# Kernel tuning notes

Measured on AMD Instinct MI355X. Metric: run time of the kernel, lower is better.

## Reference

```python
import jax, jax.numpy as jnp
import numpy as np

N_NODES = 50000
N_EDGES = 800000
D = 128
N_GRAPHS = 64
EPS = 1e-5


def _bn(x, g, b):
    # BatchNorm1d training-mode statistics over the node/graph axis
    mu = x.mean(axis=0)
    var = x.var(axis=0)
    return g * (x - mu) / jnp.sqrt(var + EPS) + b


def setup_inputs() -> dict:
    key = jax.random.key(0)
    ks = jax.random.split(key, 32)
    s = 0.05
    inp = {
        'x': jax.random.normal(ks[0], (N_NODES, D), dtype=jnp.float32),
        'edge_index': jax.random.randint(ks[1], (2, N_EDGES), 0, N_NODES, dtype=jnp.int32),
        'batch': jnp.sort(jax.random.randint(ks[2], (N_NODES,), 0, N_GRAPHS, dtype=jnp.int32)),
        # stacked ResGatedGraphConv params for 3 layers (key/query/value/skip)
        'Wk': jax.random.normal(ks[3], (3, D, D)) * s,
        'bk': jnp.zeros((3, D)),
        'Wq': jax.random.normal(ks[4], (3, D, D)) * s,
        'bq': jnp.zeros((3, D)),
        'Wv': jax.random.normal(ks[5], (3, D, D)) * s,
        'bv': jnp.zeros((3, D)),
        'Ws': jax.random.normal(ks[6], (3, D, D)) * s,
        'bs': jnp.zeros((3, D)),
        # per-layer conv BatchNorm affine params
        'g_cl': jnp.ones((3, D)), 'b_cl': jnp.zeros((3, D)),
        # pool norms
        'g_gap': jnp.ones((D,)), 'b_gap': jnp.zeros((D,)),
        'g_gsp': jnp.ones((D,)), 'b_gsp': jnp.zeros((D,)),
        # MLP head: 2*D -> 256 -> 128 -> 5
        'W1': jax.random.normal(ks[7], (2 * D, 256)) * s, 'b1': jnp.zeros((256,)),
        'g1': jnp.ones((256,)), 'bt1': jnp.zeros((256,)),
        'W2': jax.random.normal(ks[8], (256, 128)) * s, 'b2': jnp.zeros((128,)),
        'g2': jnp.ones((128,)), 'bt2': jnp.zeros((128,)),
        'Wl': jax.random.normal(ks[9], (128, 5)) * s, 'bl': jnp.zeros((5,)),
    }
    return inp


def reference(x, edge_index, batch, Wk, bk, Wq, bq, Wv, bv, Ws, bs, g_cl, b_cl,
              g_gap, b_gap, g_gsp, b_gsp, W1, b1, g1, bt1, W2, b2, g2, bt2, Wl, bl):
    src, dst = edge_index[0], edge_index[1]
    n = x.shape[0]
    for i in range(3):
        k = x @ Wk[i] + bk[i]   # target-side gate term
        q = x @ Wq[i] + bq[i]   # source-side gate term
        v = x @ Wv[i] + bv[i]   # messages
        gate = jax.nn.sigmoid(k[dst] + q[src])          # [E, D]
        agg = jax.ops.segment_sum(gate * v[src], dst, num_segments=n)
        x = agg + x @ Ws[i] + bs[i]                      # residual skip
        x = jax.nn.relu(x)
        x = _bn(x, g_cl[i], b_cl[i])
        # dropout: identity in eval mode
    counts = jax.ops.segment_sum(jnp.ones((n,), x.dtype), batch, num_segments=N_GRAPHS)
    gap = jax.ops.segment_sum(x, batch, num_segments=N_GRAPHS) / jnp.maximum(counts, 1.0)[:, None]
    gsp = jax.ops.segment_max(x, batch, num_segments=N_GRAPHS)
    gsp = jnp.where(counts[:, None] > 0, gsp, 0.0)
    gap = _bn(gap, g_gap, b_gap)
    gsp = _bn(gsp, g_gsp, b_gsp)
    out = jnp.concatenate([gap, gsp], axis=1)            # [G, 2D]
    out = _bn(jax.nn.relu(out @ W1 + b1), g1, bt1)
    out = _bn(jax.nn.relu(out @ W2 + b2), g2, bt2)
    return out @ Wl + bl                                  # [G, 5]
```

## Files before the change

### kernel.cpp

```cpp
#include <hip/hip_runtime.h>
#include <math.h>

#define N_NODES 50000
#define N_PAD 50048
#define N_EDGES 800000
#define D 128
#define N_GRAPHS 64
#define EPS 1e-5f
#define PCHUNK 16
#define GSTRIPES 8
#define SCAN_NB 196
#define NEG_LOG2E (-1.4426950408889634f)

typedef __attribute__((ext_vector_type(8))) short bf16x8;
typedef __attribute__((ext_vector_type(4))) float f32x4;
typedef __attribute__((ext_vector_type(2))) _Float16 h16x2;

static inline size_t align256(size_t x) { return (x + 255) & ~(size_t)255; }

__device__ inline unsigned short f2bf(float x) {
    unsigned u = __builtin_bit_cast(unsigned, x);
    u += 0x7FFFu + ((u >> 16) & 1u);
    return (unsigned short)(u >> 16);
}
__device__ inline float bf2f(unsigned short h) {
    unsigned u = (unsigned)h << 16;
    return __builtin_bit_cast(float, u);
}
__device__ inline unsigned short f2h(float x) {
    _Float16 h = (_Float16)x;
    return __builtin_bit_cast(unsigned short, h);
}

__global__ void prep_w(const float* __restrict__ Wk, const float* __restrict__ Wq,
                       const float* __restrict__ Wv, const float* __restrict__ Ws,
                       unsigned short* __restrict__ Whi, unsigned short* __restrict__ Wlo)
{
    const int j = blockIdx.x & 127;
    const int mat = (blockIdx.x >> 7) & 3;
    const int layer = blockIdx.x >> 9;
    const int k = threadIdx.x;
    const float* Wsrc = (mat == 0) ? Wk : (mat == 1) ? Wq : (mat == 2) ? Wv : Ws;
    const float w = Wsrc[((size_t)layer * D + k) * D + j];
    const unsigned short hi = f2bf(w);
    const unsigned short lo = f2bf(w - bf2f(hi));
    const size_t o = (((size_t)layer * 4 + mat) * D + j) * D + k;
    Whi[o] = hi;
    Wlo[o] = lo;
}

__global__ void convert_bf16(const float* __restrict__ X, unsigned short* __restrict__ Xhi)
{
    const size_t idx = (size_t)blockIdx.x * blockDim.x + threadIdx.x;
    if (idx >= (size_t)N_PAD * (D / 4)) return;
    const size_t n = idx >> 5;
    float4 v = make_float4(0.f, 0.f, 0.f, 0.f);
    if (n < N_NODES) v = ((const float4*)X)[idx];
    ((ushort4*)Xhi)[idx] = make_ushort4(f2bf(v.x), f2bf(v.y), f2bf(v.z), f2bf(v.w));
}

__global__ void gemm_kqvs_mfma(
    const unsigned short* __restrict__ Xhi,
    const unsigned short* __restrict__ Whi, const unsigned short* __restrict__ Wlo,
    const float* __restrict__ bk, const float* __restrict__ bq,
    const float* __restrict__ bv, const float* __restrict__ bs,
    float* __restrict__ Kb, unsigned short* __restrict__ QVh, float* __restrict__ Sb)
{
    const int tid = threadIdx.x;
    const int wave = tid >> 6;
    const int pair = wave & 1;
    const int ct = (wave >> 1) + 4 * blockIdx.y;
    const int colbase = ct * 16;
    const int lane = tid & 63;
    const int l16 = lane & 15;
    const int lhi = lane >> 4;

    const int mA = pair ? 1 : 0;
    const int mB = pair ? 2 : 3;

    const size_t wbA = ((size_t)mA * D + colbase + l16) * D;
    const size_t wbB = ((size_t)mB * D + colbase + l16) * D;
    bf16x8 bhA[4], blA[4], bhB[4], blB[4];
    #pragma unroll
    for (int c = 0; c < 4; ++c) {
        bhA[c] = *(const bf16x8*)(Whi + wbA + c * 32 + lhi * 8);
        blA[c] = *(const bf16x8*)(Wlo + wbA + c * 32 + lhi * 8);
        bhB[c] = *(const bf16x8*)(Whi + wbB + c * 32 + lhi * 8);
        blB[c] = *(const bf16x8*)(Wlo + wbB + c * 32 + lhi * 8);
    }

    const float biasA = (pair ? bq : bk)[colbase + l16];
    const float biasB = (pair ? bv : bs)[colbase + l16];
    const int lc = colbase + l16;
    const int rbase = blockIdx.x * (16 * GSTRIPES);

    bf16x8 an[4];
    {
        const size_t arow = (size_t)(rbase + l16) * D;
        #pragma unroll
        for (int c = 0; c < 4; ++c) an[c] = *(const bf16x8*)(Xhi + arow + c * 32 + lhi * 8);
    }
    #pragma unroll
    for (int s = 0; s < GSTRIPES; ++s) {
        bf16x8 ah[4];
        #pragma unroll
        for (int c = 0; c < 4; ++c) ah[c] = an[c];
        if (s + 1 < GSTRIPES) {
            const size_t arow = (size_t)(rbase + (s + 1) * 16 + l16) * D;
            #pragma unroll
            for (int c = 0; c < 4; ++c) an[c] = *(const bf16x8*)(Xhi + arow + c * 32 + lhi * 8);
        }
        f32x4 accA = (f32x4){0.f, 0.f, 0.f, 0.f};
        f32x4 accB = (f32x4){0.f, 0.f, 0.f, 0.f};
        #pragma unroll
        for (int c = 0; c < 4; ++c) {
            accA = __builtin_amdgcn_mfma_f32_16x16x32_bf16(ah[c], bhA[c], accA, 0, 0, 0);
            accA = __builtin_amdgcn_mfma_f32_16x16x32_bf16(ah[c], blA[c], accA, 0, 0, 0);
            accB = __builtin_amdgcn_mfma_f32_16x16x32_bf16(ah[c], bhB[c], accB, 0, 0, 0);
            accB = __builtin_amdgcn_mfma_f32_16x16x32_bf16(ah[c], blB[c], accB, 0, 0, 0);
        }
        const int r0 = rbase + s * 16;
        if (pair == 0) {
            #pragma unroll
            for (int rgi = 0; rgi < 4; ++rgi) {
                const int row = r0 + lhi * 4 + rgi;
                if (row < N_NODES) {
                    Kb[(size_t)row * D + lc] = (accA[rgi] + biasA) * NEG_LOG2E;
                    Sb[(size_t)row * D + lc] = accB[rgi] + biasB;
                }
            }
        } else {
            unsigned int* qv32 = (unsigned int*)QVh;
            #pragma unroll
            for (int rgi = 0; rgi < 4; ++rgi) {
                const int row = r0 + lhi * 4 + rgi;
                if (row < N_NODES) {
                    const unsigned qh = f2h((accA[rgi] + biasA) * NEG_LOG2E);
                    const unsigned vh = f2h(accB[rgi] + biasB);
                    qv32[(size_t)row * D + lc] = qh | (vh << 16);
                }
            }
        }
    }
}

__global__ void hist_dst(const int* __restrict__ dst, int* __restrict__ cnt) {
    int e = blockIdx.x * blockDim.x + threadIdx.x;
    if (e < N_EDGES) atomicAdd(&cnt[dst[e]], 1);
}

__global__ void scan_block_sums(const int* __restrict__ cnt, int* __restrict__ bsum) {
    __shared__ int s[256];
    const int t = threadIdx.x;
    const int i = blockIdx.x * 256 + t;
    s[t] = (i < N_NODES) ? cnt[i] : 0;
    __syncthreads();
    #pragma unroll
    for (int off = 128; off > 0; off >>= 1) {
        if (t < off) s[t] += s[t + off];
        __syncthreads();
    }
    if (t == 0) bsum[blockIdx.x] = s[0];
}

__global__ void scan_block_offsets(const int* __restrict__ bsum, int* __restrict__ boff) {
    __shared__ int s[256];
    const int t = threadIdx.x;
    s[t] = (t < SCAN_NB) ? bsum[t] : 0;
    __syncthreads();
    for (int off = 1; off < 256; off <<= 1) {
        const int add = (t >= off) ? s[t - off] : 0;
        __syncthreads();
        s[t] += add;
        __syncthreads();
    }
    if (t < SCAN_NB) boff[t] = (t == 0) ? 0 : s[t - 1];
}

__global__ void scan_final(const int* __restrict__ cnt, const int* __restrict__ boff,
                           int* __restrict__ row_start, int* __restrict__ cursor) {
    __shared__ int s[256];
    const int t = threadIdx.x;
    const int i = blockIdx.x * 256 + t;
    const int v = (i < N_NODES) ? cnt[i] : 0;
    s[t] = v;
    __syncthreads();
    for (int off = 1; off < 256; off <<= 1) {
        const int add = (t >= off) ? s[t - off] : 0;
        __syncthreads();
        s[t] += add;
        __syncthreads();
    }
    if (i < N_NODES) {
        const int excl = boff[blockIdx.x] + s[t] - v;
        row_start[i] = excl;
        cursor[i] = excl;
    }
    if (i == N_NODES - 1) {
        row_start[N_NODES] = N_EDGES;
        cursor[N_NODES] = N_EDGES;
    }
}

__global__ void fill_csr(const int* __restrict__ src, const int* __restrict__ dst,
                         int* __restrict__ cursor, int* __restrict__ col) {
    int e = blockIdx.x * blockDim.x + threadIdx.x;
    if (e < N_EDGES) {
        int d = dst[e];
        int p = atomicAdd(&cursor[d], 1);
        col[p] = src[e];
    }
}

__global__ void aggregate(const float2* __restrict__ Kb2, const uint2* __restrict__ QV2,
                          const float2* __restrict__ Sb2,
                          const int* __restrict__ row_start, const int* __restrict__ col,
                          float2* __restrict__ H2)
{
    const int wave = threadIdx.x >> 6;
    const int node = blockIdx.x * 4 + wave;
    const unsigned lane = threadIdx.x & 63;
    const size_t nb = (size_t)node * 64 + lane;
    const float2 kd = Kb2[nb];
    const float2 sb = Sb2[nb];
    float acc0 = 0.f, acc1 = 0.f;
    const int e0 = __builtin_amdgcn_readfirstlane(row_start[node]);
    const int e1 = __builtin_amdgcn_readfirstlane(row_start[node + 1]);
    int e = e0;
    for (; e + 8 <= e1; e += 8) {
        unsigned off0 = (unsigned)col[e + 0] * 64u + lane;
        unsigned off1 = (unsigned)col[e + 1] * 64u + lane;
        unsigned off2 = (unsigned)col[e + 2] * 64u + lane;
        unsigned off3 = (unsigned)col[e + 3] * 64u + lane;
        unsigned off4 = (unsigned)col[e + 4] * 64u + lane;
        unsigned off5 = (unsigned)col[e + 5] * 64u + lane;
        unsigned off6 = (unsigned)col[e + 6] * 64u + lane;
        unsigned off7 = (unsigned)col[e + 7] * 64u + lane;
        const uint2 u0 = QV2[off0];
        const uint2 u1 = QV2[off1];
        const uint2 u2 = QV2[off2];
        const uint2 u3 = QV2[off3];
        const uint2 u4 = QV2[off4];
        const uint2 u5 = QV2[off5];
        const uint2 u6 = QV2[off6];
        const uint2 u7 = QV2[off7];
        #pragma unroll
        for (int j = 0; j < 8; ++j) {
            const uint2 u = (j == 0) ? u0 : (j == 1) ? u1 : (j == 2) ? u2 : (j == 3) ? u3
                          : (j == 4) ? u4 : (j == 5) ? u5 : (j == 6) ? u6 : u7;
            const h16x2 p0 = __builtin_bit_cast(h16x2, u.x);
            const h16x2 p1 = __builtin_bit_cast(h16x2, u.y);
            acc0 = fmaf(__builtin_amdgcn_rcpf(1.0f + exp2f(kd.x + (float)p0[0])), (float)p0[1], acc0);
            acc1 = fmaf(__builtin_amdgcn_rcpf(1.0f + exp2f(kd.y + (float)p1[0])), (float)p1[1], acc1);
        }
    }
    for (; e + 4 <= e1; e += 4) {
        unsigned off0 = (unsigned)col[e + 0] * 64u + lane;
        unsigned off1 = (unsigned)col[e + 1] * 64u + lane;
        unsigned off2 = (unsigned)col[e + 2] * 64u + lane;
        unsigned off3 = (unsigned)col[e + 3] * 64u + lane;
        const uint2 u0 = QV2[off0];
        const uint2 u1 = QV2[off1];
        const uint2 u2 = QV2[off2];
        const uint2 u3 = QV2[off3];
        #pragma unroll
        for (int j = 0; j < 4; ++j) {
            const uint2 u = (j == 0) ? u0 : (j == 1) ? u1 : (j == 2) ? u2 : u3;
            const h16x2 p0 = __builtin_bit_cast(h16x2, u.x);
            const h16x2 p1 = __builtin_bit_cast(h16x2, u.y);
            acc0 = fmaf(__builtin_amdgcn_rcpf(1.0f + exp2f(kd.x + (float)p0[0])), (float)p0[1], acc0);
            acc1 = fmaf(__builtin_amdgcn_rcpf(1.0f + exp2f(kd.y + (float)p1[0])), (float)p1[1], acc1);
        }
    }
    for (; e < e1; ++e) {
        const unsigned off = (unsigned)col[e] * 64u + lane;
        const uint2 u = QV2[off];
        const h16x2 p0 = __builtin_bit_cast(h16x2, u.x);
        const h16x2 p1 = __builtin_bit_cast(h16x2, u.y);
        acc0 = fmaf(__builtin_amdgcn_rcpf(1.0f + exp2f(kd.x + (float)p0[0])), (float)p0[1], acc0);
        acc1 = fmaf(__builtin_amdgcn_rcpf(1.0f + exp2f(kd.y + (float)p1[0])), (float)p1[1], acc1);
    }
    H2[nb] = make_float2(fmaxf(acc0 + sb.x, 0.0f), fmaxf(acc1 + sb.y, 0.0f));
}

__global__ void bn_stats(const float* __restrict__ H, float* __restrict__ fsum,
                         float* __restrict__ fsq)
{
    __shared__ float s1[256], s2[256];
    const int tid = threadIdx.x;
    const int d = tid & 127;
    const int rowoff = tid >> 7;
    float sum = 0.f, sq = 0.f;
    for (int n = blockIdx.x * 2 + rowoff; n < N_NODES; n += gridDim.x * 2) {
        const float v = H[(size_t)n * D + d];
        sum += v; sq += v * v;
    }
    s1[tid] = sum; s2[tid] = sq;
    __syncthreads();
    if (tid < 128) {
        atomicAdd(&fsum[d], s1[tid] + s1[tid + 128]);
        atomicAdd(&fsq[d],  s2[tid] + s2[tid + 128]);
    }
}

__global__ void bn_apply_fused(float* __restrict__ H, const float* __restrict__ fsum,
                               const float* __restrict__ fsq, const float* __restrict__ g,
                               const float* __restrict__ b,
                               unsigned short* __restrict__ Xhi, int write_bf)
{
    const int idx = blockIdx.x * blockDim.x + threadIdx.x;
    const int total = N_NODES * D / 4;
    if (idx >= total) return;
    float4 h = ((const float4*)H)[idx];
    float hv[4] = {h.x, h.y, h.z, h.w};
    const int dbase = (idx * 4) & 127;
    float o[4];
    #pragma unroll
    for (int c = 0; c < 4; ++c) {
        const int d = dbase + c;
        const float mu = fsum[d] * (1.0f / N_NODES);
        const float var = fsq[d] * (1.0f / N_NODES) - mu * mu;
        const float sc = g[d] * rsqrtf(var + EPS);
        o[c] = (hv[c] - mu) * sc + b[d];
    }
    ((float4*)H)[idx] = make_float4(o[0], o[1], o[2], o[3]);
    if (write_bf) {
        ((ushort4*)Xhi)[idx] = make_ushort4(f2bf(o[0]), f2bf(o[1]), f2bf(o[2]), f2bf(o[3]));
    }
}

__global__ void find_gstart(const int* __restrict__ batch, int* __restrict__ gstart) {
    const int g = threadIdx.x;
    if (g > N_GRAPHS) return;
    int lo = 0, hi = N_NODES;
    while (lo < hi) {
        int mid = (lo + hi) >> 1;
        if (batch[mid] < g) lo = mid + 1; else hi = mid;
    }
    gstart[g] = lo;
}

__global__ void pool_partial(const float* __restrict__ X, const int* __restrict__ gstart,
                             float* __restrict__ psum, float* __restrict__ pmax)
{
    const int g = blockIdx.x / PCHUNK;
    const int c = blockIdx.x % PCHUNK;
    const int d = threadIdx.x;
    const int lo = gstart[g], hi = gstart[g + 1];
    float sum = 0.f, mx = -INFINITY;
    for (int n = lo + c; n < hi; n += PCHUNK) {
        const float v = X[(size_t)n * D + d];
        sum += v;
        mx = fmaxf(mx, v);
    }
    psum[(size_t)blockIdx.x * D + d] = sum;
    pmax[(size_t)blockIdx.x * D + d] = mx;
}

__global__ void pool_combine(const float* __restrict__ psum, const float* __restrict__ pmax,
                             const int* __restrict__ gstart,
                             float* __restrict__ gap, float* __restrict__ gsp)
{
    const int g = blockIdx.x;
    const int d = threadIdx.x;
    float sum = 0.f, mx = -INFINITY;
    #pragma unroll
    for (int c = 0; c < PCHUNK; ++c) {
        sum += psum[(size_t)(g * PCHUNK + c) * D + d];
        mx = fmaxf(mx, pmax[(size_t)(g * PCHUNK + c) * D + d]);
    }
    const int cnt = gstart[g + 1] - gstart[g];
    gap[g * D + d] = sum / fmaxf((float)cnt, 1.0f);
    gsp[g * D + d] = (cnt > 0) ? mx : 0.0f;
}

__global__ void bn_rows(const float* __restrict__ A, int rows, int cols,
                        const float* __restrict__ g, const float* __restrict__ b,
                        float* __restrict__ out, int out_cols, int out_off)
{
    const int c = blockIdx.x * blockDim.x + threadIdx.x;
    if (c >= cols) return;
    float sum = 0.f, sq = 0.f;
    for (int r = 0; r < rows; ++r) {
        const float v = A[r * cols + c];
        sum += v; sq += v * v;
    }
    const float mu = sum / rows;
    const float var = sq / rows - mu * mu;
    const float sc = g[c] * rsqrtf(var + EPS);
    const float sh = b[c] - mu * sc;
    for (int r = 0; r < rows; ++r) {
        out[r * out_cols + out_off + c] = A[r * cols + c] * sc + sh;
    }
}

__global__ void gemm_small(const float* __restrict__ A, const float* __restrict__ W,
                           const float* __restrict__ bias, float* __restrict__ out,
                           int K, int C, int relu)
{
    __shared__ float as[256];
    const int r = blockIdx.x;
    for (int k = threadIdx.x; k < K; k += blockDim.x) as[k] = A[r * K + k];
    __syncthreads();
    const int j = threadIdx.x;
    if (j < C) {
        float acc = bias[j];
        for (int k = 0; k < K; ++k) acc = fmaf(as[k], W[k * C + j], acc);
        if (relu) acc = fmaxf(acc, 0.f);
        out[r * C + j] = acc;
    }
}

extern "C" void kernel_launch(void* const* d_in, const int* in_sizes, int n_in,
                              void* d_out, int out_size, void* d_ws, size_t ws_size,
                              hipStream_t stream)
{
    const float* x     = (const float*)d_in[0];
    const int*   ei    = (const int*)d_in[1];
    const int*   srcE  = ei;
    const int*   dstE  = ei + N_EDGES;
    const int*   batch = (const int*)d_in[2];
    const float* Wk = (const float*)d_in[3];  const float* bk = (const float*)d_in[4];
    const float* Wq = (const float*)d_in[5];  const float* bq = (const float*)d_in[6];
    const float* Wv = (const float*)d_in[7];  const float* bv = (const float*)d_in[8];
    const float* Ws = (const float*)d_in[9];  const float* bs = (const float*)d_in[10];
    const float* g_cl = (const float*)d_in[11]; const float* b_cl = (const float*)d_in[12];
    const float* g_gap = (const float*)d_in[13]; const float* b_gap = (const float*)d_in[14];
    const float* g_gsp = (const float*)d_in[15]; const float* b_gsp = (const float*)d_in[16];
    const float* W1 = (const float*)d_in[17]; const float* b1 = (const float*)d_in[18];
    const float* g1 = (const float*)d_in[19]; const float* bt1 = (const float*)d_in[20];
    const float* W2 = (const float*)d_in[21]; const float* b2 = (const float*)d_in[22];
    const float* g2 = (const float*)d_in[23]; const float* bt2 = (const float*)d_in[24];
    const float* Wl = (const float*)d_in[25]; const float* bl = (const float*)d_in[26];
    float* out = (float*)d_out;

    char* ws = (char*)d_ws;
    size_t off = 0;
    const size_t bufB = (size_t)N_NODES * D * sizeof(float);
    float* Kb = (float*)(ws + off); off = align256(off + bufB);
    unsigned short* QVh = (unsigned short*)(ws + off); off = align256(off + bufB);
    float* Sb = (float*)(ws + off); off = align256(off + bufB);
    float* H  = (float*)(ws + off); off = align256(off + bufB);
    unsigned short* Xhi = (unsigned short*)(ws + off); off = align256(off + (size_t)N_PAD * D * 2);
    unsigned short* Whi = (unsigned short*)(ws + off); off = align256(off + (size_t)12 * D * D * 2);
    unsigned short* Wlo = (unsigned short*)(ws + off); off = align256(off + (size_t)12 * D * D * 2);
    float* fsum = (float*)(ws + off); off = align256(off + 128 * sizeof(float));
    float* fsq  = (float*)(ws + off); off = align256(off + 128 * sizeof(float));
    int* cnt       = (int*)(ws + off); off = align256(off + (size_t)N_NODES * sizeof(int));
    int* row_start = (int*)(ws + off); off = align256(off + (size_t)(N_NODES + 1) * sizeof(int));
    int* cursor    = (int*)(ws + off); off = align256(off + (size_t)(N_NODES + 1) * sizeof(int));
    int* colI      = (int*)(ws + off); off = align256(off + (size_t)N_EDGES * sizeof(int));
    int* bsum      = (int*)(ws + off); off = align256(off + 256 * sizeof(int));
    int* boff      = (int*)(ws + off); off = align256(off + 256 * sizeof(int));
    int* gstart    = (int*)(ws + off); off = align256(off + (N_GRAPHS + 1) * sizeof(int));
    float* psum = (float*)(ws + off); off = align256(off + (size_t)N_GRAPHS * PCHUNK * D * sizeof(float));
    float* pmax = (float*)(ws + off); off = align256(off + (size_t)N_GRAPHS * PCHUNK * D * sizeof(float));
    float* gap = (float*)(ws + off); off = align256(off + (size_t)N_GRAPHS * D * sizeof(float));
    float* gsp = (float*)(ws + off); off = align256(off + (size_t)N_GRAPHS * D * sizeof(float));
    float* h0  = (float*)(ws + off); off = align256(off + (size_t)N_GRAPHS * 256 * sizeof(float));
    float* h1  = (float*)(ws + off); off = align256(off + (size_t)N_GRAPHS * 256 * sizeof(float));
    float* h2  = (float*)(ws + off); off = align256(off + (size_t)N_GRAPHS * 128 * sizeof(float));
    if (off > ws_size) return;

    hipMemsetAsync(cnt, 0, (size_t)N_NODES * sizeof(int), stream);
    hist_dst<<<(N_EDGES + 255) / 256, 256, 0, stream>>>(dstE, cnt);
    scan_block_sums<<<SCAN_NB, 256, 0, stream>>>(cnt, bsum);
    scan_block_offsets<<<1, 256, 0, stream>>>(bsum, boff);
    scan_final<<<SCAN_NB, 256, 0, stream>>>(cnt, boff, row_start, cursor);
    fill_csr<<<(N_EDGES + 255) / 256, 256, 0, stream>>>(srcE, dstE, cursor, colI);
    find_gstart<<<1, 128, 0, stream>>>(batch, gstart);
    prep_w<<<12 * 128, 128, 0, stream>>>(Wk, Wq, Wv, Ws, Whi, Wlo);
    convert_bf16<<<(N_PAD * (D / 4) + 255) / 256, 256, 0, stream>>>(x, Xhi);

    for (int i = 0; i < 3; ++i) {
        gemm_kqvs_mfma<<<dim3(N_PAD / (16 * GSTRIPES), 2), 512, 0, stream>>>(
            Xhi,
            Whi + (size_t)i * 4 * D * D, Wlo + (size_t)i * 4 * D * D,
            bk + i * D, bq + i * D, bv + i * D, bs + i * D,
            Kb, QVh, Sb);
        aggregate<<<N_NODES / 4, 256, 0, stream>>>(
            (const float2*)Kb, (const uint2*)QVh, (const float2*)Sb, row_start, colI, (float2*)H);
        hipMemsetAsync(fsum, 0, 128 * sizeof(float), stream);
        hipMemsetAsync(fsq, 0, 128 * sizeof(float), stream);
        bn_stats<<<256, 256, 0, stream>>>(H, fsum, fsq);
        bn_apply_fused<<<(N_NODES * D / 4 + 255) / 256, 256, 0, stream>>>(
            H, fsum, fsq, g_cl + i * D, b_cl + i * D, Xhi, (i < 2) ? 1 : 0);
    }

    pool_partial<<<N_GRAPHS * PCHUNK, 128, 0, stream>>>(H, gstart, psum, pmax);
    pool_combine<<<N_GRAPHS, 128, 0, stream>>>(psum, pmax, gstart, gap, gsp);
    bn_rows<<<1, 128, 0, stream>>>(gap, N_GRAPHS, 128, g_gap, b_gap, h0, 256, 0);
    bn_rows<<<1, 128, 0, stream>>>(gsp, N_GRAPHS, 128, g_gsp, b_gsp, h0, 256, 128);

    gemm_small<<<N_GRAPHS, 256, 0, stream>>>(h0, W1, b1, h1, 256, 256, 1);
    bn_rows<<<1, 256, 0, stream>>>(h1, N_GRAPHS, 256, g1, bt1, h1, 256, 0);
    gemm_small<<<N_GRAPHS, 256, 0, stream>>>(h1, W2, b2, h2, 256, 128, 1);
    bn_rows<<<1, 128, 0, stream>>>(h2, N_GRAPHS, 128, g2, bt2, h2, 128, 0);
    gemm_small<<<N_GRAPHS, 256, 0, stream>>>(h2, Wl, bl, out, 128, 5, 0);
}
```

Baseline: 731.0 us.

## Split wave into half-waves processing two edges per gather with 16-byte loads

The aggregate kernel now has each half-wave (32 lanes) handle a different source edge, with each lane gathering a 16-byte packed K/Q/V slice covering four feature dims instead of 8 bytes for two. The partial sums from the two halves are combined with a cross-half shuffle before the skip add and ReLU. bn_stats is also vectorised to float4 loads with a deeper shared-memory reduction. The intent is to halve the number of gather instructions and widen memory transactions, at the cost of extra shuffles, an odd-edge tail where the upper half-wave sits idle, and more registers per lane.

```diff
diff --git a/kernel.cpp b/kernel.cpp
--- a/kernel.cpp
+++ b/kernel.cpp
@@ -212,94 +212,107 @@
     }
 }
 
-__global__ void aggregate(const float2* __restrict__ Kb2, const uint2* __restrict__ QV2,
-                          const float2* __restrict__ Sb2,
+__global__ void aggregate(const float4* __restrict__ Kb4, const uint4* __restrict__ QV4,
+                          const float4* __restrict__ Sb4,
                           const int* __restrict__ row_start, const int* __restrict__ col,
-                          float2* __restrict__ H2)
+                          float4* __restrict__ H4)
 {
     const int wave = threadIdx.x >> 6;
     const int node = blockIdx.x * 4 + wave;
     const unsigned lane = threadIdx.x & 63;
-    const size_t nb = (size_t)node * 64 + lane;
-    const float2 kd = Kb2[nb];
-    const float2 sb = Sb2[nb];
-    float acc0 = 0.f, acc1 = 0.f;
+    const unsigned l31 = lane & 31;
+    const bool hi = lane >= 32;
+    const size_t nb = (size_t)node * 32 + l31;
+    const float4 kd = Kb4[nb];
+    float a0 = 0.f, a1 = 0.f, a2 = 0.f, a3 = 0.f;
     const int e0 = __builtin_amdgcn_readfirstlane(row_start[node]);
     const int e1 = __builtin_amdgcn_readfirstlane(row_start[node + 1]);
     int e = e0;
+
+#define AGG_DIM(u, comp, kdc, acc)                                              \
+    {                                                                           \
+        const h16x2 p = __builtin_bit_cast(h16x2, (u).comp);                    \
+        acc = fmaf(__builtin_amdgcn_rcpf(1.0f + exp2f(kdc + (float)p[0])),      \
+                   (float)p[1], acc);                                           \
+    }
+#define AGG_EDGE(u) AGG_DIM(u, x, kd.x, a0) AGG_DIM(u, y, kd.y, a1) \
+                    AGG_DIM(u, z, kd.z, a2) AGG_DIM(u, w, kd.w, a3)
+
     for (; e + 8 <= e1; e += 8) {
-        unsigned off0 = (unsigned)col[e + 0] * 64u + lane;
-        unsigned off1 = (unsigned)col[e + 1] * 64u + lane;
-        unsigned off2 = (unsigned)col[e + 2] * 64u + lane;
-        unsigned off3 = (unsigned)col[e + 3] * 64u + lane;
-        unsigned off4 = (unsigned)col[e + 4] * 64u + lane;
-        unsigned off5 = (unsigned)col[e + 5] * 64u + lane;
-        unsigned off6 = (unsigned)col[e + 6] * 64u + lane;
-        unsigned off7 = (unsigned)col[e + 7] * 64u + lane;
-        const uint2 u0 = QV2[off0];
-        const uint2 u1 = QV2[off1];
-        const uint2 u2 = QV2[off2];
-        const uint2 u3 = QV2[off3];
-        const uint2 u4 = QV2[off4];
-        const uint2 u5 = QV2[off5];
-        const uint2 u6 = QV2[off6];
-        const uint2 u7 = QV2[off7];
+        const int s0 = col[e + 0], s1 = col[e + 1], s2 = col[e + 2], s3 = col[e + 3];
+        const int s4 = col[e + 4], s5 = col[e + 5], s6 = col[e + 6], s7 = col[e + 7];
+        const unsigned o0 = (unsigned)(hi ? s1 : s0) * 32u + l31;
+        const unsigned o1 = (unsigned)(hi ? s3 : s2) * 32u + l31;
+        const unsigned o2 = (unsigned)(hi ? s5 : s4) * 32u + l31;
+        const unsigned o3 = (unsigned)(hi ? s7 : s6) * 32u + l31;
+        const uint4 u0 = QV4[o0];
+        const uint4 u1 = QV4[o1];
+        const uint4 u2 = QV4[o2];
+        const uint4 u3 = QV4[o3];
+        AGG_EDGE(u0) AGG_EDGE(u1) AGG_EDGE(u2) AGG_EDGE(u3)
+    }
+    for (; e + 2 <= e1; e += 2) {
+        const int s0 = col[e + 0], s1 = col[e + 1];
+        const unsigned o = (unsigned)(hi ? s1 : s0) * 32u + l31;
+        const uint4 u = QV4[o];
+        AGG_EDGE(u)
+    }
+    if (e < e1 && !hi) {
+        const unsigned o = (unsigned)col[e] * 32u + l31;
+        const uint4 u = QV4[o];
+        AGG_EDGE(u)
+    }
+#undef AGG_EDGE
+#undef AGG_DIM
+
+    a0 += __shfl_xor(a0, 32);
+    a1 += __shfl_xor(a1, 32);
+    a2 += __shfl_xor(a2, 32);
+    a3 += __shfl_xor(a3, 32);
+    if (!hi) {
+        const float4 sb = Sb4[nb];
+        H4[nb] = make_float4(fmaxf(a0 + sb.x, 0.0f), fmaxf(a1 + sb.y, 0.0f),
+                             fmaxf(a2 + sb.z, 0.0f), fmaxf(a3 + sb.w, 0.0f));
+    }
+}
+
+__global__ void bn_stats(const float4* __restrict__ H4, float* __restrict__ fsum,
+                         float* __restrict__ fsq)
+{
+    __shared__ float s1[256][4];
+    __shared__ float s2[256][4];
+    const int tid = threadIdx.x;
+    const int dgrp = tid & 31;
+    const int rowg = tid >> 5;
+    float sm0 = 0.f, sm1 = 0.f, sm2 = 0.f, sm3 = 0.f;
+    float q0 = 0.f, q1 = 0.f, q2 = 0.f, q3 = 0.f;
+    for (int n = blockIdx.x * 8 + rowg; n < N_NODES; n += gridDim.x * 8) {
+        const float4 v = H4[(size_t)n * 32 + dgrp];
+        sm0 += v.x; sm1 += v.y; sm2 += v.z; sm3 += v.w;
+        q0 = fmaf(v.x, v.x, q0); q1 = fmaf(v.y, v.y, q1);
+        q2 = fmaf(v.z, v.z, q2); q3 = fmaf(v.w, v.w, q3);
+    }
+    s1[tid][0] = sm0; s1[tid][1] = sm1; s1[tid][2] = sm2; s1[tid][3] = sm3;
+    s2[tid][0] = q0;  s2[tid][1] = q1;  s2[tid][2] = q2;  s2[tid][3] = q3;
+    __syncthreads();
+    if (tid < 128) {
         #pragma unroll
-        for (int j = 0; j < 8; ++j) {
-            const uint2 u = (j == 0) ? u0 : (j == 1) ? u1 : (j == 2) ? u2 : (j == 3) ? u3
-                          : (j == 4) ? u4 : (j == 5) ? u5 : (j == 6) ? u6 : u7;
-            const h16x2 p0 = __builtin_bit_cast(h16x2, u.x);
-            const h16x2 p1 = __builtin_bit_cast(h16x2, u.y);
-            acc0 = fmaf(__builtin_amdgcn_rcpf(1.0f + exp2f(kd.x + (float)p0[0])), (float)p0[1], acc0);
-            acc1 = fmaf(__builtin_amdgcn_rcpf(1.0f + exp2f(kd.y + (float)p1[0])), (float)p1[1], acc1);
+        for (int c = 0; c < 4; ++c) { s1[tid][c] += s1[tid + 128][c]; s2[tid][c] += s2[tid + 128][c]; }
+    }
+    __syncthreads();
+    if (tid < 64) {
+        #pragma unroll
+        for (int c = 0; c < 4; ++c) { s1[tid][c] += s1[tid + 64][c]; s2[tid][c] += s2[tid + 64][c]; }
+    }
+    __syncthreads();
+    if (tid < 32) {
+        #pragma unroll
+        for (int c = 0; c < 4; ++c) {
+            const float fs = s1[tid][c] + s1[tid + 32][c];
+            const float fq = s2[tid][c] + s2[tid + 32][c];
+            atomicAdd(&fsum[tid * 4 + c], fs);
+            atomicAdd(&fsq[tid * 4 + c], fq);
         }
-    }
-    for (; e + 4 <= e1; e += 4) {
-        unsigned off0 = (unsigned)col[e + 0] * 64u + lane;
-        unsigned off1 = (unsigned)col[e + 1] * 64u + lane;
-        unsigned off2 = (unsigned)col[e + 2] * 64u + lane;
-        unsigned off3 = (unsigned)col[e + 3] * 64u + lane;
-        const uint2 u0 = QV2[off0];
-        const uint2 u1 = QV2[off1];
-        const uint2 u2 = QV2[off2];
-        const uint2 u3 = QV2[off3];
-        #pragma unroll
-        for (int j = 0; j < 4; ++j) {
-            const uint2 u = (j == 0) ? u0 : (j == 1) ? u1 : (j == 2) ? u2 : u3;
-            const h16x2 p0 = __builtin_bit_cast(h16x2, u.x);
-            const h16x2 p1 = __builtin_bit_cast(h16x2, u.y);
-            acc0 = fmaf(__builtin_amdgcn_rcpf(1.0f + exp2f(kd.x + (float)p0[0])), (float)p0[1], acc0);
-            acc1 = fmaf(__builtin_amdgcn_rcpf(1.0f + exp2f(kd.y + (float)p1[0])), (float)p1[1], acc1);
-        }
-    }
-    for (; e < e1; ++e) {
-        const unsigned off = (unsigned)col[e] * 64u + lane;
-        const uint2 u = QV2[off];
-        const h16x2 p0 = __builtin_bit_cast(h16x2, u.x);
-        const h16x2 p1 = __builtin_bit_cast(h16x2, u.y);
-        acc0 = fmaf(__builtin_amdgcn_rcpf(1.0f + exp2f(kd.x + (float)p0[0])), (float)p0[1], acc0);
-        acc1 = fmaf(__builtin_amdgcn_rcpf(1.0f + exp2f(kd.y + (float)p1[0])), (float)p1[1], acc1);
-    }
-    H2[nb] = make_float2(fmaxf(acc0 + sb.x, 0.0f), fmaxf(acc1 + sb.y, 0.0f));
-}
-
-__global__ void bn_stats(const float* __restrict__ H, float* __restrict__ fsum,
-                         float* __restrict__ fsq)
-{
-    __shared__ float s1[256], s2[256];
-    const int tid = threadIdx.x;
-    const int d = tid & 127;
-    const int rowoff = tid >> 7;
-    float sum = 0.f, sq = 0.f;
-    for (int n = blockIdx.x * 2 + rowoff; n < N_NODES; n += gridDim.x * 2) {
-        const float v = H[(size_t)n * D + d];
-        sum += v; sq += v * v;
-    }
-    s1[tid] = sum; s2[tid] = sq;
-    __syncthreads();
-    if (tid < 128) {
-        atomicAdd(&fsum[d], s1[tid] + s1[tid + 128]);
-        atomicAdd(&fsq[d],  s2[tid] + s2[tid + 128]);
     }
 }
 
@@ -479,10 +492,10 @@
             bk + i * D, bq + i * D, bv + i * D, bs + i * D,
             Kb, QVh, Sb);
         aggregate<<<N_NODES / 4, 256, 0, stream>>>(
-            (const float2*)Kb, (const uint2*)QVh, (const float2*)Sb, row_start, colI, (float2*)H);
+            (const float4*)Kb, (const uint4*)QVh, (const float4*)Sb, row_start, colI, (float4*)H);
         hipMemsetAsync(fsum, 0, 128 * sizeof(float), stream);
         hipMemsetAsync(fsq, 0, 128 * sizeof(float), stream);
-        bn_stats<<<256, 256, 0, stream>>>(H, fsum, fsq);
+        bn_stats<<<256, 256, 0, stream>>>((const float4*)H, fsum, fsq);
         bn_apply_fused<<<(N_NODES * D / 4 + 255) / 256, 256, 0, stream>>>(
             H, fsum, fsq, g_cl + i * D, b_cl + i * D, Xhi, (i < 2) ? 1 : 0);
     }
```

Result: no change. 742.4 us (+1.6%).
